# Performance work log

Measured on AMD Instinct MI355X. Metric: run time of the kernel, lower is better.

Reference implementation:

```python
import jax, jax.numpy as jnp
import numpy as np

B, T, D = 256, 200, 32          # batch, time steps, input_size
H, PH, PREP = 512, 256, 16      # hidden_size, p_hidden, prep_hidden
COV, COVH, CLFH = 32, 128, 64   # cov_size, cov_hidden, classification_hidden
DT = 0.05                       # euler step size


def setup_inputs() -> dict:
    key = jax.random.key(0)
    ks = jax.random.split(key, 32)
    n = lambda k, shape, s=0.02: (s * jax.random.normal(k, shape)).astype(jnp.float32)
    inp = {}
    inp["cov"] = jax.random.normal(ks[0], (B, COV), dtype=jnp.float32)
    inp["X"] = jax.random.normal(ks[1], (T, B, D), dtype=jnp.float32)
    inp["M"] = (jax.random.uniform(ks[2], (T, B, D)) < 0.3).astype(jnp.float32)
    # covariates_mapping: Linear(COV,COVH) -> ReLU -> Linear(COVH,H) -> Tanh
    inp["Wc1"] = n(ks[3], (COVH, COV), 0.1); inp["bc1"] = jnp.full((COVH,), 0.05, jnp.float32)
    inp["Wc2"] = n(ks[4], (H, COVH), 0.1);   inp["bc2"] = jnp.full((H,), 0.05, jnp.float32)
    # GRUODECell: three bias-free Linear(H,H)
    inp["Whr"] = n(ks[5], (H, H), 0.05)
    inp["Whz"] = n(ks[6], (H, H), 0.05)
    inp["Whh"] = n(ks[7], (H, H), 0.05)
    # log_normal_dist: Linear(H,PH) -> ReLU -> Linear(PH, 2D)
    inp["Wp1"] = n(ks[8], (PH, H), 0.05);  inp["bp1"] = jnp.full((PH,), 0.05, jnp.float32)
    inp["Wp2"] = n(ks[9], (2 * D, PH), 0.05); inp["bp2"] = jnp.full((2 * D,), 0.05, jnp.float32)
    # GRUObsCell prep params
    std = np.sqrt(2.0 / (4 + PREP))
    inp["w_prep"] = (std * jax.random.normal(ks[10], (D, 4, PREP))).astype(jnp.float32)
    inp["bias_prep"] = jnp.full((D, PREP), 0.1, jnp.float32)
    # torch GRUCell(PREP*D, H): gates ordered (r, z, n)
    inp["W_ih"] = n(ks[11], (3 * H, PREP * D), 0.05)
    inp["W_hh"] = n(ks[12], (3 * H, H), 0.05)
    inp["b_ih"] = jnp.zeros((3 * H,), jnp.float32)
    inp["b_hh"] = jnp.zeros((3 * H,), jnp.float32)
    # classifier: Linear(H,CLFH) -> ReLU -> Linear(CLFH,1)
    inp["Wclf1"] = n(ks[13], (CLFH, H), 0.05); inp["bclf1"] = jnp.full((CLFH,), 0.05, jnp.float32)
    inp["Wclf2"] = n(ks[14], (1, CLFH), 0.05); inp["bclf2"] = jnp.full((1,), 0.05, jnp.float32)
    return inp


def reference(cov, X, M, Wc1, bc1, Wc2, bc2, Whr, Whz, Whh, Wp1, bp1, Wp2, bp2,
              w_prep, bias_prep, W_ih, W_hh, b_ih, b_hh, Wclf1, bclf1, Wclf2, bclf2):
    # initial hidden state from covariates
    h0 = jnp.tanh(jax.nn.relu(cov @ Wc1.T + bc1) @ Wc2.T + bc2)  # [B,H]

    def step(h, inp):
        Xt, Mt = inp  # [B,D], [B,D]
        # autonomous GRU-ODE euler step (impute=False -> zero input x)
        r = jax.nn.sigmoid(h @ Whr.T)
        z = jax.nn.sigmoid(h @ Whz.T)
        u = jnp.tanh((r * h) @ Whh.T)
        h = h + DT * (1.0 - z) * (u - h)
        # log-normal observation distribution from hidden state
        p = jax.nn.relu(h @ Wp1.T + bp1) @ Wp2.T + bp2  # [B,2D]
        mean, logvar = jnp.split(p, 2, axis=1)
        sigma = jnp.exp(0.5 * logvar)
        err = (Xt - mean) / sigma
        # per-feature preprocessing: [B,D,4] x [D,4,PREP] -> [B,D,PREP]
        stacked = jnp.stack([Xt, mean, logvar, err], axis=2)
        gi = jax.nn.relu(jnp.einsum('bdf,dfp->bdp', stacked, w_prep) + bias_prep)
        gi = (gi * Mt[:, :, None]).reshape(Xt.shape[0], -1)  # [B, D*PREP]
        # torch GRUCell update (gates r,z,n)
        gx = gi @ W_ih.T + b_ih
        gh = h @ W_hh.T + b_hh
        xr, xz, xn = jnp.split(gx, 3, axis=1)
        hr, hz, hn = jnp.split(gh, 3, axis=1)
        rg = jax.nn.sigmoid(xr + hr)
        zg = jax.nn.sigmoid(xz + hz)
        ng = jnp.tanh(xn + rg * hn)
        h_new = (1.0 - zg) * ng + zg * h
        # scatter-style update: only rows with at least one observation (i_obs)
        obs = (jnp.sum(Mt, axis=1) > 0.0)[:, None]
        h = jnp.where(obs, h_new, h)
        return h, h

    _, h_path = jax.lax.scan(step, h0, (X, M))  # [T,B,H]
    preds = jax.nn.relu(h_path @ Wclf1.T + bclf1) @ Wclf2.T + bclf2  # [T,B,1]
    return preds
```

## Files before the change

kernel.cpp:

```cpp
#include <hip/hip_runtime.h>
#include <hip/hip_bf16.h>

constexpr int Bn = 256, Tn = 200, Dn = 32, Hn = 512, PHn = 256, PREPn = 16;
constexpr int COVn = 32, COVHn = 128, CLFHn = 64;
constexpr float DTc = 0.05f;
constexpr int NT = 512;

constexpr int CSTR = 32;
constexpr int NLINES = 64;

typedef _Float16 h2v __attribute__((ext_vector_type(2)));
typedef _Float16 f16x8 __attribute__((ext_vector_type(8)));
typedef float f32x4 __attribute__((ext_vector_type(4)));

constexpr int PK_WP1   = 0;
constexpr int PK_WP2   = 131072;
constexpr int PK_WCLF1 = 147456;
constexpr int PK_TOTAL = 180224;

constexpr size_t WS_ACT = 393216;
constexpr size_t WS_OBS = 4587520;
constexpr size_t WS_BAR = 4591616;

__device__ __forceinline__ float sigmoidf(float x) { return 1.0f / (1.0f + __expf(-x)); }

__device__ __forceinline__ float fdot2(unsigned w, unsigned v, float acc) {
#if __has_builtin(__builtin_amdgcn_fdot2)
  return __builtin_amdgcn_fdot2(__builtin_bit_cast(h2v, w),
                                __builtin_bit_cast(h2v, v), acc, false);
#else
  h2v a = __builtin_bit_cast(h2v, w), b = __builtin_bit_cast(h2v, v);
  return acc + (float)a.x * (float)b.x + (float)a.y * (float)b.y;
#endif
}
__device__ __forceinline__ float dotq(uint4 w, uint4 h, float acc) {
  acc = fdot2(w.x, h.x, acc); acc = fdot2(w.y, h.y, acc);
  acc = fdot2(w.z, h.z, acc); acc = fdot2(w.w, h.w, acc);
  return acc;
}
__device__ __forceinline__ unsigned pack2(float a, float b) {
  h2v h; h.x = (_Float16)a; h.y = (_Float16)b;
  return __builtin_bit_cast(unsigned, h);
}

__device__ __forceinline__ void cohS(unsigned long long* p, unsigned long long v) {
  __hip_atomic_store(p, v, __ATOMIC_RELAXED, __HIP_MEMORY_SCOPE_SYSTEM);
}
__device__ __forceinline__ void cohSf(float* p, float v) {
  __hip_atomic_store(p, v, __ATOMIC_RELAXED, __HIP_MEMORY_SCOPE_SYSTEM);
}

__device__ __forceinline__ void bar_arrive(unsigned* ctrs, int line) {
  __syncthreads();
  if (threadIdx.x == 0)
    __hip_atomic_fetch_add(&ctrs[line * CSTR], 1u,
                           __ATOMIC_RELAXED, __HIP_MEMORY_SCOPE_AGENT);
}
__device__ __forceinline__ void bar_wait(unsigned* ctrs, int rg, unsigned& ep) {
  ep += 1;
  const unsigned target = ep * 64u;
  if (threadIdx.x < 16) {
    const unsigned* myc = &ctrs[(rg * 16 + threadIdx.x) * CSTR];
    for (;;) {
      unsigned s = __hip_atomic_load(myc, __ATOMIC_RELAXED, __HIP_MEMORY_SCOPE_AGENT);
      #pragma unroll
      for (int o = 8; o; o >>= 1) s += __shfl_down(s, o, 16);
      s = __shfl(s, 0, 16);
      if (s >= target) break;
      __builtin_amdgcn_s_sleep(1);
    }
  }
  __syncthreads();
}

struct PrepArgs { const float *Wp1, *Wp2, *Wclf1; _Float16* dst; unsigned* bar; };

__global__ void prep_pack_kernel(PrepArgs a) {
  const int idx = blockIdx.x * 256 + threadIdx.x;
  if (idx < NLINES * CSTR) a.bar[idx] = 0u;
  if (idx >= PK_TOTAL) return;
  int off, N, K; const float* src;
  if      (idx < PK_WP2)   { off = PK_WP1;   N = 256; K = 512; src = a.Wp1; }
  else if (idx < PK_WCLF1) { off = PK_WP2;   N = 64;  K = 256; src = a.Wp2; }
  else                     { off = PK_WCLF1; N = 64;  K = 512; src = a.Wclf1; }
  const int li = idx - off, e = li & 7, t2 = li >> 3, j = t2 % N, k8 = t2 / N;
  a.dst[idx] = (_Float16)src[(size_t)j * K + k8 * 8 + e];
}

struct CoopArgs {
  const float *cov, *X, *M;
  const float *Wc1, *bc1, *Wc2, *bc2;
  const float *Whr, *Whz, *Whh;
  const float *bp1, *bp2;
  const float *w_prep, *bias_prep;
  const float *W_ih, *W_hh, *b_ih, *b_hh;
  const float *bclf1, *Wclf2, *bclf2;
  const uint4 *Wp1Q, *Wp2Q, *Wclf1Q;
  char* act;
  float* obs;
  unsigned* bar;
  float* out;
};

__global__ __launch_bounds__(NT)
void gruode_coop(CoopArgs a) {
  const int bid = blockIdx.x, tid = threadIdx.x;
  const int cg = bid >> 2, rg = bid & 3;
  const int g = rg * 64 + cg;
  const int c_loc = tid >> 6, r_loc = tid & 63;
  const int c = cg * 8 + c_loc;
  const int lane = tid & 63, wv = tid >> 6;
  const int mt = wv & 3, kh = wv >> 2;
  const int line = rg * 16 + (cg & 15);
  const int rgofs = rg * 64;

  __shared__ __align__(16) uint4 Wrz16[16 * 64];
  __shared__ __align__(16) uint4 Wxrz16[16 * 64];
  __shared__ __align__(16) uint4 Whrz16[16 * 64];
  __shared__ __align__(16) uint4 Whh8[8 * 64];
  __shared__ __align__(16) uint4 Wxn8[8 * 64];
  __shared__ __align__(16) uint4 Whn8[8 * 64];
  __shared__ __align__(16) uint4 stageQ[64 * 64];
  __shared__ float redQ[2][64][17];
  __shared__ __align__(16) uint4 hrowQ[64];
  __shared__ __align__(16) uint4 qrowQ[32];
  __shared__ __align__(8)  _Float16 outH[512];
  __shared__ __align__(8)  _Float16 giH[512];
  __shared__ float bp1L[PHn], bp2L[2 * Dn], pL[2 * Dn];
  __shared__ float xrowL[Dn], mrowL[Dn];
  __shared__ float bclfL[CLFHn], wclf2L[CLFHn], bgL[48];
  __shared__ float obsL[64];

  unsigned long long* outU = (unsigned long long*)outH;
  unsigned long long* giU  = (unsigned long long*)giH;

  auto slabp = [&](int arr, int buf) -> uint4* {
    return (uint4*)(a.act + ((size_t)(arr * 4 + buf) << 18));
  };

  float hfull;
  {
    float* covF = (float*)redQ;
    float* midF = (float*)stageQ;
    for (int i = tid; i < 64 * 32; i += NT)
      covF[i] = a.cov[(size_t)rgofs * COVn + i];
    __syncthreads();
    for (int i = tid; i < 64 * 128; i += NT) {
      const int rr = i >> 7, m = i & 127;
      float acc = a.bc1[m];
      #pragma unroll 8
      for (int k = 0; k < COVn; ++k) acc += covF[rr * 32 + k] * a.Wc1[m * COVn + k];
      midF[i] = fmaxf(acc, 0.0f);
    }
    __syncthreads();
    {
      float acc = a.bc2[c];
      const float* w2 = a.Wc2 + (size_t)c * COVHn;
      #pragma unroll 4
      for (int k = 0; k < COVHn; ++k) acc += midF[r_loc * 128 + k] * w2[k];
      hfull = tanhf(acc);
      outH[r_loc * 8 + c_loc] = (_Float16)hfull;
    }
    __syncthreads();
    unsigned long long* hA3u = (unsigned long long*)slabp(0, 3);
    const size_t oub0 = (size_t)(cg * 256 + rgofs) * 2;
    if (tid < 128) cohS(&hA3u[oub0 + tid], outU[tid]);
    __syncthreads();
  }

  for (int nfo = tid; nfo < 4608; nfo += NT) {
    int li; const float* srow; uint4* dst;
    if (nfo < 3072) {
      li = nfo & 1023; const int seg = nfo >> 10;
      const int n = li >> 6;
      const int col = cg * 8 + (n & 7);
      if (seg == 0)      { srow = (n < 8 ? a.Whr : a.Whz) + (size_t)col * Hn; dst = Wrz16; }
      else if (seg == 1) { srow = a.W_ih + (size_t)((n < 8 ? 0 : Hn) + col) * Hn; dst = Wxrz16; }
      else               { srow = a.W_hh + (size_t)((n < 8 ? 0 : Hn) + col) * Hn; dst = Whrz16; }
    } else {
      li = (nfo - 3072) & 511; const int seg = (nfo - 3072) >> 9;
      const int n = li >> 6; const int col = cg * 8 + n;
      if (seg == 0)      { srow = a.Whh + (size_t)col * Hn; dst = Whh8; }
      else if (seg == 1) { srow = a.W_ih + (size_t)(2 * Hn + col) * Hn; dst = Wxn8; }
      else               { srow = a.W_hh + (size_t)(2 * Hn + col) * Hn; dst = Whn8; }
    }
    const int q = li & 63;
    const float* s8 = srow + q * 8;
    uint4 u;
    u.x = pack2(s8[0], s8[1]); u.y = pack2(s8[2], s8[3]);
    u.z = pack2(s8[4], s8[5]); u.w = pack2(s8[6], s8[7]);
    dst[li] = u;
  }
  if (tid < PHn)    bp1L[tid] = a.bp1[tid];
  if (tid < 2 * Dn) bp2L[tid] = a.bp2[tid];
  if (tid < CLFHn)  { bclfL[tid] = a.bclf1[tid]; wclf2L[tid] = a.Wclf2[tid]; }
  if (tid < 48) {
    const int cl = tid / 6, rem = tid % 6, gate = rem >> 1, s = rem & 1;
    const int j = gate * Hn + cg * 8 + cl;
    bgL[tid] = s ? a.b_hh[j] : a.b_ih[j];
  }
  const float bclf2r = a.bclf2[0];

  unsigned ep = 0;
  bar_arrive(a.bar, line); bar_wait(a.bar, rg, ep);

  float zz = 0.f, hbc = 0.f;
  const size_t oub = (size_t)(cg * 256 + rgofs) * 2;

  auto stage_fill = [&](const uint4* A) {
    #pragma unroll
    for (int i = 0; i < 8; ++i) {
      const int idx = tid + i * NT;
      stageQ[idx] = A[(size_t)(idx >> 6) * 256 + rgofs + (idx & 63)];
    }
  };

  auto ldA = [&](int ks) -> f16x8 {
    return __builtin_bit_cast(f16x8,
        stageQ[(4 * ks + (lane >> 4)) * 64 + mt * 16 + (lane & 15)]);
  };
  auto mma_wide = [&](const uint4* Bw) -> f32x4 {
    f32x4 acc = {0.f, 0.f, 0.f, 0.f};
    #pragma unroll
    for (int i = 0; i < 8; ++i) {
      const int ks = kh * 8 + i;
      const f16x8 bv = __builtin_bit_cast(f16x8, Bw[(lane & 15) * 64 + ks * 4 + (lane >> 4)]);
      acc = __builtin_amdgcn_mfma_f32_16x16x32_f16(ldA(ks), bv, acc, 0, 0, 0);
    }
    return acc;
  };
  auto mma_half = [&](const uint4* Bw) -> f32x4 {
    f32x4 acc = {0.f, 0.f, 0.f, 0.f};
    const int n = lane & 15;
    #pragma unroll
    for (int i = 0; i < 8; ++i) {
      const int ks = kh * 8 + i;
      uint4 ub = {0u, 0u, 0u, 0u};
      if (n < 8) ub = Bw[n * 64 + ks * 4 + (lane >> 4)];
      acc = __builtin_amdgcn_mfma_f32_16x16x32_f16(ldA(ks), __builtin_bit_cast(f16x8, ub),
                                                   acc, 0, 0, 0);
    }
    return acc;
  };
  auto redw = [&](f32x4 acc) {
    const int col = lane & 15, r0 = mt * 16 + ((lane >> 4) << 2);
    #pragma unroll
    for (int j = 0; j < 4; ++j) redQ[kh][r0 + j][col] = acc[j];
  };

  auto do_clf = [&](const uint4* hAbase, int tout) {
    if (tid < CLFHn) {
      hrowQ[tid] = hAbase[(size_t)tid * 256 + g];
      float acc = bclfL[tid];
      #pragma unroll 8
      for (int q = 0; q < Hn / 8; ++q) acc = dotq(a.Wclf1Q[q * CLFHn + tid], hrowQ[q], acc);
      float cc = fmaxf(acc, 0.0f) * wclf2L[tid];
      #pragma unroll
      for (int o = 32; o; o >>= 1) cc += __shfl_down(cc, o, 64);
      if (tid == 0) a.out[tout * Bn + g] = cc + bclf2r;
    }
  };

  for (int t = 0; t < Tn; ++t) {
    if ((t & 3) == 0) __builtin_amdgcn_fence(__ATOMIC_ACQUIRE, "agent");

    const int bs = t & 3, bp = (t + 3) & 3;
    const uint4* hA_prev = slabp(0, bp);
    uint4* rh_cur = slabp(1, bs);
    uint4* hB_cur = slabp(2, bs);
    uint4* gi_cur = slabp(3, bs);
    uint4* hA_cur = slabp(0, bs);
    float* obs_cur = a.obs + bs * 256;

    stage_fill(hA_prev);
    __syncthreads();
    redw(mma_wide(Wrz16));
    __syncthreads();
    {
      const float sr = redQ[0][r_loc][c_loc]     + redQ[1][r_loc][c_loc];
      const float sz = redQ[0][r_loc][c_loc + 8] + redQ[1][r_loc][c_loc + 8];
      const float rr = sigmoidf(sr);
      zz = sigmoidf(sz);
      outH[r_loc * 8 + c_loc] = (_Float16)(rr * hfull);
    }
    __syncthreads();
    if (tid < 128) cohS(((unsigned long long*)rh_cur) + oub + tid, outU[tid]);
    bar_arrive(a.bar, line);
    if (t > 0) do_clf(hA_prev, t - 1);
    bar_wait(a.bar, rg, ep);

    stage_fill(rh_cur);
    __syncthreads();
    redw(mma_half(Whh8));
    __syncthreads();
    {
      const float su = redQ[0][r_loc][c_loc] + redQ[1][r_loc][c_loc];
      const float u = tanhf(su);
      hbc = hfull + DTc * (1.0f - zz) * (u - hfull);
      outH[r_loc * 8 + c_loc] = (_Float16)hbc;
    }
    __syncthreads();
    if (tid < 128) cohS(((unsigned long long*)hB_cur) + oub + tid, outU[tid]);
    bar_arrive(a.bar, line);
    if (tid >= 64 && tid < 96)        xrowL[tid - 64] = a.X[((size_t)t * Bn + g) * Dn + (tid - 64)];
    else if (tid >= 96 && tid < 128)  mrowL[tid - 96] = a.M[((size_t)t * Bn + g) * Dn + (tid - 96)];
    bar_wait(a.bar, rg, ep);

    if (tid < 64) hrowQ[tid] = hB_cur[(size_t)tid * 256 + g];
    __syncthreads();
    if (tid < PHn) {
      float a0 = bp1L[tid], a1 = 0.f;
      #pragma unroll 8
      for (int q = 0; q < Hn / 8; q += 2) {
        a0 = dotq(a.Wp1Q[q * PHn + tid], hrowQ[q], a0);
        a1 = dotq(a.Wp1Q[(q + 1) * PHn + tid], hrowQ[q + 1], a1);
      }
      ((_Float16*)qrowQ)[tid] = (_Float16)fmaxf(a0 + a1, 0.0f);
    }
    __syncthreads();
    if (tid < 2 * Dn) {
      float acc = bp2L[tid];
      #pragma unroll 4
      for (int q = 0; q < PHn / 8; ++q)
        acc = dotq(a.Wp2Q[q * (2 * Dn) + tid], qrowQ[q], acc);
      pL[tid] = acc;
    }
    __syncthreads();
    {
      const int d = tid >> 4, pp = tid & 15;
      const float xv   = xrowL[d];
      const float mean = pL[d];
      const float logv = pL[Dn + d];
      const float err  = (xv - mean) * __expf(-0.5f * logv);
      float acc = a.bias_prep[d * PREPn + pp];
      acc += xv   * a.w_prep[(d * 4 + 0) * PREPn + pp];
      acc += mean * a.w_prep[(d * 4 + 1) * PREPn + pp];
      acc += logv * a.w_prep[(d * 4 + 2) * PREPn + pp];
      acc += err  * a.w_prep[(d * 4 + 3) * PREPn + pp];
      giH[tid] = (_Float16)(fmaxf(acc, 0.0f) * mrowL[d]);
      if (tid < 32) {
        const unsigned long long bb = __ballot(mrowL[tid] > 0.0f);
        if (tid == 0) cohSf(&obs_cur[g], bb ? 1.0f : 0.0f);
      }
    }
    __syncthreads();
    if (tid < 128)
      cohS(((unsigned long long*)gi_cur) + (size_t)(tid >> 1) * 512 + g * 2 + (tid & 1), giU[tid]);
    bar_arrive(a.bar, line);

    stage_fill(hB_cur);
    __syncthreads();
    redw(mma_wide(Whrz16));
    __syncthreads();
    const float hr = redQ[0][r_loc][c_loc]     + redQ[1][r_loc][c_loc];
    const float hz = redQ[0][r_loc][c_loc + 8] + redQ[1][r_loc][c_loc + 8];
    __syncthreads();
    redw(mma_half(Whn8));
    __syncthreads();
    const float hn = redQ[0][r_loc][c_loc] + redQ[1][r_loc][c_loc];
    bar_wait(a.bar, rg, ep);

    stage_fill(gi_cur);
    if (tid < 64) obsL[tid] = obs_cur[rgofs + tid];
    __syncthreads();
    redw(mma_wide(Wxrz16));
    __syncthreads();
    const float xr = redQ[0][r_loc][c_loc]     + redQ[1][r_loc][c_loc];
    const float xz = redQ[0][r_loc][c_loc + 8] + redQ[1][r_loc][c_loc + 8];
    __syncthreads();
    redw(mma_half(Wxn8));
    __syncthreads();
    {
      const float xn  = redQ[0][r_loc][c_loc] + redQ[1][r_loc][c_loc];
      const float rgg = sigmoidf(xr + hr + bgL[c_loc * 6 + 0] + bgL[c_loc * 6 + 1]);
      const float zgg = sigmoidf(xz + hz + bgL[c_loc * 6 + 2] + bgL[c_loc * 6 + 3]);
      const float ng  = tanhf(xn + bgL[c_loc * 6 + 4] + rgg * (hn + bgL[c_loc * 6 + 5]));
      hfull = (obsL[r_loc] > 0.0f) ? ((1.0f - zgg) * ng + zgg * hbc) : hbc;
      outH[r_loc * 8 + c_loc] = (_Float16)hfull;
    }
    __syncthreads();
    if (tid < 128) cohS(((unsigned long long*)hA_cur) + oub + tid, outU[tid]);
    bar_arrive(a.bar, line);
    bar_wait(a.bar, rg, ep);
  }

  do_clf(slabp(0, (Tn - 1) & 3), Tn - 1);
}

extern "C" void kernel_launch(void* const* d_in, const int* in_sizes, int n_in,
                              void* d_out, int out_size, void* d_ws, size_t ws_size,
                              hipStream_t stream) {
  char* ws = (char*)d_ws;

  CoopArgs a;
  a.cov  = (const float*)d_in[0];
  a.X    = (const float*)d_in[1];
  a.M    = (const float*)d_in[2];
  a.Wc1  = (const float*)d_in[3];  a.bc1 = (const float*)d_in[4];
  a.Wc2  = (const float*)d_in[5];  a.bc2 = (const float*)d_in[6];
  a.Whr  = (const float*)d_in[7];  a.Whz = (const float*)d_in[8];  a.Whh = (const float*)d_in[9];
  const float* Wp1 = (const float*)d_in[10]; a.bp1 = (const float*)d_in[11];
  const float* Wp2 = (const float*)d_in[12]; a.bp2 = (const float*)d_in[13];
  a.w_prep = (const float*)d_in[14]; a.bias_prep = (const float*)d_in[15];
  a.W_ih = (const float*)d_in[16]; a.W_hh = (const float*)d_in[17];
  a.b_ih = (const float*)d_in[18]; a.b_hh = (const float*)d_in[19];
  const float* Wclf1 = (const float*)d_in[20]; a.bclf1 = (const float*)d_in[21];
  a.Wclf2 = (const float*)d_in[22]; a.bclf2 = (const float*)d_in[23];

  _Float16* pk = (_Float16*)ws;
  a.Wp1Q   = (const uint4*)(pk + PK_WP1);
  a.Wp2Q   = (const uint4*)(pk + PK_WP2);
  a.Wclf1Q = (const uint4*)(pk + PK_WCLF1);
  a.act = ws + WS_ACT;
  a.obs = (float*)(ws + WS_OBS);
  a.bar = (unsigned*)(ws + WS_BAR);
  a.out = (float*)d_out;

  PrepArgs p;
  p.Wp1 = Wp1; p.Wp2 = Wp2; p.Wclf1 = Wclf1;
  p.dst = pk; p.bar = a.bar;
  prep_pack_kernel<<<(PK_TOTAL + 255) / 256, 256, 0, stream>>>(p);
  gruode_coop<<<Bn, NT, 0, stream>>>(a);
}
```

Before: 5.689 ms.

## Pad GRU weight smem layout and merge rz/n gate MFMAs per wave group

Stores the per-block GRU weight tiles in LDS with a padded (q*17+n / q*9+n) layout so B-operand reads by MFMA lanes avoid bank conflicts. It also replaces the two-pass split-K scheme (wide rz pass then half n pass, each reduced across two k-halves) with a single pass: waves 0-3 compute the r/z gates over full K while waves 4-7 compute the n gate over full K. This removes two __syncthreads and a reduction add per phase. The cost is a longer serial MFMA chain per wave and imbalanced useful work, since the n-gate waves zero half their B lanes.

```diff
diff --git a/kernel.cpp b/kernel.cpp
--- a/kernel.cpp
+++ b/kernel.cpp
@@ -111,15 +111,16 @@
   const int c = cg * 8 + c_loc;
   const int lane = tid & 63, wv = tid >> 6;
   const int mt = wv & 3, kh = wv >> 2;
+  const int pp4 = wv >> 2;
   const int line = rg * 16 + (cg & 15);
   const int rgofs = rg * 64;
 
-  __shared__ __align__(16) uint4 Wrz16[16 * 64];
-  __shared__ __align__(16) uint4 Wxrz16[16 * 64];
-  __shared__ __align__(16) uint4 Whrz16[16 * 64];
-  __shared__ __align__(16) uint4 Whh8[8 * 64];
-  __shared__ __align__(16) uint4 Wxn8[8 * 64];
-  __shared__ __align__(16) uint4 Whn8[8 * 64];
+  __shared__ __align__(16) uint4 Wrz16[64 * 17];
+  __shared__ __align__(16) uint4 Wxrz16[64 * 17];
+  __shared__ __align__(16) uint4 Whrz16[64 * 17];
+  __shared__ __align__(16) uint4 Whh8[64 * 9];
+  __shared__ __align__(16) uint4 Wxn8[64 * 9];
+  __shared__ __align__(16) uint4 Whn8[64 * 9];
   __shared__ __align__(16) uint4 stageQ[64 * 64];
   __shared__ float redQ[2][64][17];
   __shared__ __align__(16) uint4 hrowQ[64];
@@ -169,27 +170,34 @@
   }
 
   for (int nfo = tid; nfo < 4608; nfo += NT) {
-    int li; const float* srow; uint4* dst;
+    int li; const float* srow; uint4* dst; int phys;
     if (nfo < 3072) {
       li = nfo & 1023; const int seg = nfo >> 10;
-      const int n = li >> 6;
+      const int n = li >> 6, q = li & 63;
       const int col = cg * 8 + (n & 7);
       if (seg == 0)      { srow = (n < 8 ? a.Whr : a.Whz) + (size_t)col * Hn; dst = Wrz16; }
       else if (seg == 1) { srow = a.W_ih + (size_t)((n < 8 ? 0 : Hn) + col) * Hn; dst = Wxrz16; }
       else               { srow = a.W_hh + (size_t)((n < 8 ? 0 : Hn) + col) * Hn; dst = Whrz16; }
+      phys = q * 17 + n;
+      const float* s8 = srow + q * 8;
+      uint4 u;
+      u.x = pack2(s8[0], s8[1]); u.y = pack2(s8[2], s8[3]);
+      u.z = pack2(s8[4], s8[5]); u.w = pack2(s8[6], s8[7]);
+      dst[phys] = u;
     } else {
       li = (nfo - 3072) & 511; const int seg = (nfo - 3072) >> 9;
-      const int n = li >> 6; const int col = cg * 8 + n;
+      const int n = li >> 6, q = li & 63;
+      const int col = cg * 8 + n;
       if (seg == 0)      { srow = a.Whh + (size_t)col * Hn; dst = Whh8; }
       else if (seg == 1) { srow = a.W_ih + (size_t)(2 * Hn + col) * Hn; dst = Wxn8; }
       else               { srow = a.W_hh + (size_t)(2 * Hn + col) * Hn; dst = Whn8; }
-    }
-    const int q = li & 63;
-    const float* s8 = srow + q * 8;
-    uint4 u;
-    u.x = pack2(s8[0], s8[1]); u.y = pack2(s8[2], s8[3]);
-    u.z = pack2(s8[4], s8[5]); u.w = pack2(s8[6], s8[7]);
-    dst[li] = u;
+      phys = q * 9 + n;
+      const float* s8 = srow + q * 8;
+      uint4 u;
+      u.x = pack2(s8[0], s8[1]); u.y = pack2(s8[2], s8[3]);
+      u.z = pack2(s8[4], s8[5]); u.w = pack2(s8[6], s8[7]);
+      dst[phys] = u;
+    }
   }
   if (tid < PHn)    bp1L[tid] = a.bp1[tid];
   if (tid < 2 * Dn) bp2L[tid] = a.bp2[tid];
@@ -221,22 +229,23 @@
   };
   auto mma_wide = [&](const uint4* Bw) -> f32x4 {
     f32x4 acc = {0.f, 0.f, 0.f, 0.f};
+    const int n = lane & 15, l4 = lane >> 4;
     #pragma unroll
     for (int i = 0; i < 8; ++i) {
       const int ks = kh * 8 + i;
-      const f16x8 bv = __builtin_bit_cast(f16x8, Bw[(lane & 15) * 64 + ks * 4 + (lane >> 4)]);
+      const f16x8 bv = __builtin_bit_cast(f16x8, Bw[(ks * 4 + l4) * 17 + n]);
       acc = __builtin_amdgcn_mfma_f32_16x16x32_f16(ldA(ks), bv, acc, 0, 0, 0);
     }
     return acc;
   };
   auto mma_half = [&](const uint4* Bw) -> f32x4 {
     f32x4 acc = {0.f, 0.f, 0.f, 0.f};
-    const int n = lane & 15;
+    const int n = lane & 15, l4 = lane >> 4;
     #pragma unroll
     for (int i = 0; i < 8; ++i) {
       const int ks = kh * 8 + i;
       uint4 ub = {0u, 0u, 0u, 0u};
-      if (n < 8) ub = Bw[n * 64 + ks * 4 + (lane >> 4)];
+      if (n < 8) ub = Bw[(ks * 4 + l4) * 9 + n];
       acc = __builtin_amdgcn_mfma_f32_16x16x32_f16(ldA(ks), __builtin_bit_cast(f16x8, ub),
                                                    acc, 0, 0, 0);
     }
@@ -246,6 +255,21 @@
     const int col = lane & 15, r0 = mt * 16 + ((lane >> 4) << 2);
     #pragma unroll
     for (int j = 0; j < 4; ++j) redQ[kh][r0 + j][col] = acc[j];
+  };
+  auto mma_p4 = [&](const uint4* Bw16, const uint4* Bw9) {
+    f32x4 acc = {0.f, 0.f, 0.f, 0.f};
+    const int n = lane & 15, l4 = lane >> 4;
+    #pragma unroll
+    for (int ks = 0; ks < 16; ++ks) {
+      uint4 ub = {0u, 0u, 0u, 0u};
+      if (pp4 == 0)      ub = Bw16[(ks * 4 + l4) * 17 + n];
+      else if (n < 8)    ub = Bw9[(ks * 4 + l4) * 9 + n];
+      acc = __builtin_amdgcn_mfma_f32_16x16x32_f16(ldA(ks), __builtin_bit_cast(f16x8, ub),
+                                                   acc, 0, 0, 0);
+    }
+    const int col = lane & 15, r0 = mt * 16 + ((lane >> 4) << 2);
+    #pragma unroll
+    for (int j = 0; j < 4; ++j) redQ[pp4][r0 + j][col] = acc[j];
   };
 
   auto do_clf = [&](const uint4* hAbase, int tout) {
@@ -350,28 +374,22 @@
 
     stage_fill(hB_cur);
     __syncthreads();
-    redw(mma_wide(Whrz16));
-    __syncthreads();
-    const float hr = redQ[0][r_loc][c_loc]     + redQ[1][r_loc][c_loc];
-    const float hz = redQ[0][r_loc][c_loc + 8] + redQ[1][r_loc][c_loc + 8];
-    __syncthreads();
-    redw(mma_half(Whn8));
-    __syncthreads();
-    const float hn = redQ[0][r_loc][c_loc] + redQ[1][r_loc][c_loc];
+    mma_p4(Whrz16, Whn8);
+    __syncthreads();
+    const float hr = redQ[0][r_loc][c_loc];
+    const float hz = redQ[0][r_loc][c_loc + 8];
+    const float hn = redQ[1][r_loc][c_loc];
     bar_wait(a.bar, rg, ep);
 
     stage_fill(gi_cur);
     if (tid < 64) obsL[tid] = obs_cur[rgofs + tid];
     __syncthreads();
-    redw(mma_wide(Wxrz16));
-    __syncthreads();
-    const float xr = redQ[0][r_loc][c_loc]     + redQ[1][r_loc][c_loc];
-    const float xz = redQ[0][r_loc][c_loc + 8] + redQ[1][r_loc][c_loc + 8];
-    __syncthreads();
-    redw(mma_half(Wxn8));
+    mma_p4(Wxrz16, Wxn8);
     __syncthreads();
     {
-      const float xn  = redQ[0][r_loc][c_loc] + redQ[1][r_loc][c_loc];
+      const float xr = redQ[0][r_loc][c_loc];
+      const float xz = redQ[0][r_loc][c_loc + 8];
+      const float xn = redQ[1][r_loc][c_loc];
       const float rgg = sigmoidf(xr + hr + bgL[c_loc * 6 + 0] + bgL[c_loc * 6 + 1]);
       const float zgg = sigmoidf(xz + hz + bgL[c_loc * 6 + 2] + bgL[c_loc * 6 + 3]);
       const float ng  = tanhf(xn + bgL[c_loc * 6 + 4] + rgg * (hn + bgL[c_loc * 6 + 5]));
```

Measured after the change: 5.172 ms. -9.1%, faster.
